# Optimization experiments

Hardware: AMD Instinct MI355X
Metric: run time of the kernel (lower is better)

The kernel has to match this reference:

```python
import jax, jax.numpy as jnp
import numpy as np

N_OBJ = 4096
IN_DIM = 1024
OUT_DIM = 1024
H = OUT_DIM // 2  # per-direction hidden, BidirectionalTreeLSTM uses out_dim//2
L = 2             # num_layer


def _build_tree(n):
    # balanced binary heap tree: node i has children 2i+1, 2i+2
    left = np.array([2 * i + 1 if 2 * i + 1 < n else -1 for i in range(n)], np.int32)
    right = np.array([2 * i + 2 if 2 * i + 2 < n else -1 for i in range(n)], np.int32)
    parent = np.full(n, -1, np.int32)
    for i in range(n):
        if left[i] >= 0:
            parent[left[i]] = i
        if right[i] >= 0:
            parent[right[i]] = i
    post, stack = [], [(0, False)]
    while stack:
        node, seen = stack.pop()
        if node < 0:
            continue
        if seen:
            post.append(node)
        else:
            stack.append((node, True))
            stack.append((int(right[node]), False))
            stack.append((int(left[node]), False))
    pre, stack = [], [0]
    while stack:
        node = stack.pop()
        if node < 0:
            continue
        pre.append(node)
        stack.append(int(right[node]))
        stack.append(int(left[node]))
    pad = lambda a: np.where(a < 0, n, a).astype(np.int32)  # slot n = zeros (no child/parent)
    return (np.array(post, np.int32), np.array(pre, np.int32),
            pad(left), pad(right), pad(parent))


def setup_inputs() -> dict:
    key = jax.random.key(0)
    ks = jax.random.split(key, 8)
    post, pre, left, right, parent = _build_tree(N_OBJ)

    def w(k, shape, fan_in):
        return jax.random.normal(k, shape, jnp.float32) * np.float32(1.0 / np.sqrt(fan_in))

    # bias init per the torch module: forget-gate blocks get constants, rest zero
    fw_bl = np.zeros((L, 6 * H), np.float32); fw_bl[:, 2 * H:4 * H] = 0.5
    fw_br = fw_bl.copy()
    bw_bh = np.zeros((L, 5 * H), np.float32); bw_bh[:, 2 * H:3 * H] = 1.0

    return {
        "features": jax.random.normal(ks[0], (N_OBJ, IN_DIM), jnp.float32),
        "fw_Wp": w(ks[1], (L, H, IN_DIM), IN_DIM),
        "fw_bp": jnp.zeros((L, H), jnp.float32),
        "fw_Wx": w(ks[2], (L, 6 * H, IN_DIM), IN_DIM),
        "fw_bx": jnp.zeros((L, 6 * H), jnp.float32),
        "fw_Wl": w(ks[3], (L, 6 * H, H), H),
        "fw_bl": jnp.asarray(fw_bl),
        "fw_Wr": w(ks[4], (L, 6 * H, H), H),
        "fw_br": jnp.asarray(fw_br),
        "bw_Wp": w(ks[5], (L, H, IN_DIM), IN_DIM),
        "bw_bp": jnp.zeros((L, H), jnp.float32),
        "bw_Wx": w(ks[6], (L, 5 * H, IN_DIM), IN_DIM),
        "bw_bx": jnp.zeros((L, 5 * H), jnp.float32),
        "bw_Wh": w(ks[7], (L, 5 * H, H), H),
        "bw_bh": jnp.asarray(bw_bh),
        "post_order": jnp.asarray(post),
        "pre_order": jnp.asarray(pre),
        "left_child": jnp.asarray(left),
        "right_child": jnp.asarray(right),
        "parent": jnp.asarray(parent),
    }


def _tree_leaves_to_root(feats, Wp, bp, Wx, bx, Wl, bl, Wr, br,
                         post_order, left_child, right_child):
    n = feats.shape[0]
    h = bp.shape[0]
    px = feats @ Wp.T + bp   # [n, h]   -- self path
    x2 = feats @ Wx.T + bx   # [n, 6h]  -- gate input, batched once

    def step(carry, idx):
        cbuf, hbuf = carry   # [n+1, h]; row n is permanent zero slot for missing children
        lc = left_child[idx]
        rc = right_child[idx]
        g = x2[idx] + hbuf[lc] @ Wl.T + bl + hbuf[rc] @ Wr.T + br
        i, o, fl, fr, u, r = jnp.split(g, 6)
        i = jax.nn.sigmoid(i); o = jax.nn.sigmoid(o)
        fl = jax.nn.sigmoid(fl); fr = jax.nn.sigmoid(fr)
        u = jnp.tanh(u); r = jax.nn.sigmoid(r)
        c = i * u + fl * cbuf[lc] + fr * cbuf[rc]
        hc = o * jnp.tanh(c)
        hf = r * hc + (1.0 - r) * px[idx]   # highway mix
        return (cbuf.at[idx].set(c), hbuf.at[idx].set(hf)), None

    init = (jnp.zeros((n + 1, h), feats.dtype), jnp.zeros((n + 1, h), feats.dtype))
    (_, hbuf), _ = jax.lax.scan(step, init, post_order)
    return hbuf[:n]


def _tree_root_to_leaves(feats, Wp, bp, Wx, bx, Wh, bh, pre_order, parent):
    n = feats.shape[0]
    h = bp.shape[0]
    px = feats @ Wp.T + bp   # [n, h]
    x2 = feats @ Wx.T + bx   # [n, 5h]

    def step(carry, idx):
        cbuf, hbuf = carry
        p = parent[idx]      # root maps to zero slot n -> iofuh(0) == bias, as in torch
        g = x2[idx] + hbuf[p] @ Wh.T + bh
        i, o, f, u, r = jnp.split(g, 5)
        i = jax.nn.sigmoid(i); o = jax.nn.sigmoid(o)
        f = jax.nn.sigmoid(f); u = jnp.tanh(u); r = jax.nn.sigmoid(r)
        c = i * u + f * cbuf[p]
        hc = o * jnp.tanh(c)
        hf = r * hc + (1.0 - r) * px[idx]
        return (cbuf.at[idx].set(c), hbuf.at[idx].set(hf)), None

    init = (jnp.zeros((n + 1, h), feats.dtype), jnp.zeros((n + 1, h), feats.dtype))
    (_, hbuf), _ = jax.lax.scan(step, init, pre_order)
    return hbuf[:n]


def reference(features, fw_Wp, fw_bp, fw_Wx, fw_bx, fw_Wl, fw_bl, fw_Wr, fw_br,
              bw_Wp, bw_bp, bw_Wx, bw_bx, bw_Wh, bw_bh,
              post_order, pre_order, left_child, right_child, parent):
    feats = features
    for l in range(L):  # MultiLayer_BTreeLSTM: stacked bidirectional layers
        h_fwd = _tree_leaves_to_root(feats, fw_Wp[l], fw_bp[l], fw_Wx[l], fw_bx[l],
                                     fw_Wl[l], fw_bl[l], fw_Wr[l], fw_br[l],
                                     post_order, left_child, right_child)
        h_bwd = _tree_root_to_leaves(feats, bw_Wp[l], bw_bp[l], bw_Wx[l], bw_bx[l],
                                     bw_Wh[l], bw_bh[l], pre_order, parent)
        feats = jnp.concatenate([h_fwd, h_bwd], axis=1)  # [n, out_dim]
    return feats
```

## Files before the change

kernel.cpp:

```cpp
#include <hip/hip_runtime.h>
#include <cstdint>
#include <cstddef>


#define HDIM 512
#define ZROW 4096
#define NCAT 6656

typedef _Float16 f16;
typedef f16   f16x8 __attribute__((ext_vector_type(8)));
typedef float f32x4 __attribute__((ext_vector_type(4)));

__device__ __forceinline__ float sigm(float x) { return 1.0f / (1.0f + expf(-x)); }

__device__ __forceinline__ void glds16(const f16* g, f16* l)
{
    __builtin_amdgcn_global_load_lds(
        (const __attribute__((address_space(1))) void*)g,
        (__attribute__((address_space(3))) void*)l,
        16, 0, 0);
}

__global__ __launch_bounds__(256) void cvt16(
    const float* __restrict__ s, f16* __restrict__ d, int n8)
{
    int i = blockIdx.x * 256 + threadIdx.x;
    if (i >= n8) return;
    float4 v0 = ((const float4*)s)[(size_t)i * 2];
    float4 v1 = ((const float4*)s)[(size_t)i * 2 + 1];
    f16x8 o;
    o[0] = (f16)v0.x; o[1] = (f16)v0.y; o[2] = (f16)v0.z; o[3] = (f16)v0.w;
    o[4] = (f16)v1.x; o[5] = (f16)v1.y; o[6] = (f16)v1.z; o[7] = (f16)v1.w;
    *(f16x8*)(d + (size_t)i * 8) = o;
}

__global__ __launch_bounds__(256) void cvt16_lr(
    const float* __restrict__ Wl, const float* __restrict__ Wr, f16* __restrict__ d)
{
    int i = blockIdx.x * 256 + threadIdx.x;
    int col8 = (i * 8) & 1023;
    int row  = (i * 8) >> 10;
    const float* s = (col8 < HDIM) ? (Wl + (size_t)row * HDIM + col8)
                                   : (Wr + (size_t)row * HDIM + col8 - HDIM);
    float4 v0 = ((const float4*)s)[0];
    float4 v1 = ((const float4*)s)[1];
    f16x8 o;
    o[0] = (f16)v0.x; o[1] = (f16)v0.y; o[2] = (f16)v0.z; o[3] = (f16)v0.w;
    o[4] = (f16)v1.x; o[5] = (f16)v1.y; o[6] = (f16)v1.z; o[7] = (f16)v1.w;
    int np = (row & 511) * 6 + (row >> 9);
    *(f16x8*)(d + (size_t)np * 1024 + col8) = o;
}

__global__ __launch_bounds__(256) void cvt16_perm5(
    const float* __restrict__ s, f16* __restrict__ d)
{
    int i = blockIdx.x * 256 + threadIdx.x;
    int col8 = (i * 8) & 511;
    int row  = (i * 8) >> 9;
    float4 v0 = ((const float4*)(s + (size_t)row * HDIM + col8))[0];
    float4 v1 = ((const float4*)(s + (size_t)row * HDIM + col8))[1];
    f16x8 o;
    o[0] = (f16)v0.x; o[1] = (f16)v0.y; o[2] = (f16)v0.z; o[3] = (f16)v0.w;
    o[4] = (f16)v1.x; o[5] = (f16)v1.y; o[6] = (f16)v1.z; o[7] = (f16)v1.w;
    int np = (row & 511) * 5 + (row >> 9);
    *(f16x8*)(d + (size_t)np * HDIM + col8) = o;
}

__global__ __launch_bounds__(256) void biascat_k(
    const float* __restrict__ a, const float* __restrict__ b,
    const float* __restrict__ c, const float* __restrict__ dd,
    float* __restrict__ o)
{
    int t = blockIdx.x * 256 + threadIdx.x;
    if (t >= NCAT) return;
    float v;
    if (t < 512) v = a[t];
    else if (t < 3584) v = b[t - 512];
    else if (t < 4096) v = c[t - 3584];
    else v = dd[t - 4096];
    o[t] = v;
}

__global__ void zero_slots(f16* H, float* cbf, float* cbb)
{
    int t = threadIdx.x;
    H[(size_t)ZROW * 1024 + t] = (f16)0.0f;
    if (t < HDIM) {
        cbf[(size_t)ZROW * HDIM + t] = 0.0f;
        cbb[(size_t)ZROW * HDIM + t] = 0.0f;
    }
}

__global__ __launch_bounds__(256) void mm_pre(
    const f16* __restrict__ A, const f16* __restrict__ W,
    const float* __restrict__ bias, f16* __restrict__ C, int N, int K)
{
    __shared__ __align__(16) f16 Ab[2][128 * 32];
    __shared__ __align__(16) f16 Bb[2][128 * 32];
    const int t  = threadIdx.x;
    const int L  = t & 63;
    const int w  = t >> 6;
    const int wm = (w & 1) << 6;
    const int wn = (w >> 1) << 6;
    const int fr = L & 15;
    const int fq = L >> 4;
    const int la  = L >> 2;
    const int cs  = (((L & 3) ^ ((L >> 3) & 3)) << 3);

    const f16* a0 = A + (size_t)(blockIdx.y * 128 + w * 16 + la) * K + cs;
    const f16* a1 = a0 + (size_t)64 * K;
    const f16* b0 = W + (size_t)(blockIdx.x * 128 + w * 16 + la) * K + cs;
    const f16* b1 = b0 + (size_t)64 * K;
    const int lo = w * 512 + L * 8;
    const int hi = lo + 2048;

    f32x4 acc[4][4] = {};
    const int nt = K >> 5;

#define STG_P(sel, k0)                       \
    do {                                     \
        glds16(a0 + (k0), &Ab[sel][lo]);     \
        glds16(a1 + (k0), &Ab[sel][hi]);     \
        glds16(b0 + (k0), &Bb[sel][lo]);     \
        glds16(b1 + (k0), &Bb[sel][hi]);     \
    } while (0)

    STG_P(0, 0);
    __syncthreads();
    int cur = 0;
    const int fsw = ((fr >> 1) & 3) << 3;
    for (int tt = 0; tt < nt; ++tt) {
        if (tt + 1 < nt) STG_P(cur ^ 1, (tt + 1) << 5);
        f16x8 af[4], bg[4];
#pragma unroll
        for (int i = 0; i < 4; ++i)
            af[i] = *(const f16x8*)(&Ab[cur][(wm + i * 16 + fr) * 32 + ((fq << 3) ^ fsw)]);
#pragma unroll
        for (int j = 0; j < 4; ++j)
            bg[j] = *(const f16x8*)(&Bb[cur][(wn + j * 16 + fr) * 32 + ((fq << 3) ^ fsw)]);
#pragma unroll
        for (int i = 0; i < 4; ++i)
#pragma unroll
            for (int j = 0; j < 4; ++j)
                acc[i][j] = __builtin_amdgcn_mfma_f32_16x16x32_f16(
                    af[i], bg[j], acc[i][j], 0, 0, 0);
        __syncthreads();
        cur ^= 1;
    }
#undef STG_P

    const int gr0 = blockIdx.y * 128 + wm + fq * 4;
    const int gc0 = blockIdx.x * 128 + wn + fr;
#pragma unroll
    for (int j = 0; j < 4; ++j) {
        const int gc = gc0 + j * 16;
        const float bj = bias[gc];
#pragma unroll
        for (int i = 0; i < 4; ++i) {
            const int gr = gr0 + i * 16;
#pragma unroll
            for (int rr = 0; rr < 4; ++rr)
                C[(size_t)(gr + rr) * N + gc] = (f16)(acc[i][j][rr] + bj);
        }
    }
}

__global__ __launch_bounds__(256) void stage_fused(
    const f16* __restrict__ Wlr, const f16* __restrict__ Wh,
    f16* H, const f16* __restrict__ PX,
    const int* __restrict__ lc, const int* __restrict__ rc,
    const int* __restrict__ par,
    int fbase, int fm, int bbase, int bm,
    float* __restrict__ cbf, float* __restrict__ cbb,
    float* out32,
    const float* __restrict__ bl, const float* __restrict__ br,
    const float* __restrict__ bh)
{
    __shared__ __align__(16) char smem[57344];
    f16*   Ab0 = (f16*)smem;
    f16*   Bb0 = (f16*)(smem + 32768);
    float* Sg  = (float*)smem;

    const int t   = threadIdx.x;
    const int L   = t & 63;
    const int w   = t >> 6;
    const int fr  = L & 15;
    const int fq  = L >> 4;
    const int rch = L >> 3;
    const int cs  = (((L & 7) ^ rch) << 3);
    const int fsw = (fr & 7) << 3;
    const int nfB = ((fm + 127) >> 7) * 32;

    if ((int)blockIdx.x < nfB) {
        const int by = blockIdx.x >> 5;
        const int bx = blockIdx.x & 31;
        const int wm = (w & 1) << 6;
        const int wn = (w >> 1) * 48;

        const f16* aLo[4]; const f16* aHi[4];
#pragma unroll
        for (int cc = 0; cc < 4; ++cc) {
            int g  = by * 128 + (w * 4 + cc) * 8 + rch;
            int n1 = ZROW, n2 = ZROW;
            if (g < fm) { n1 = lc[fbase + g]; n2 = rc[fbase + g]; }
            aLo[cc] = H + (size_t)n1 * 1024 + cs;
            aHi[cc] = H + (size_t)n2 * 1024 + cs - HDIM;
        }
        const f16* bsrc[3];
#pragma unroll
        for (int cc = 0; cc < 3; ++cc)
            bsrc[cc] = Wlr + (size_t)(bx * 96 + (w * 3 + cc) * 8 + rch) * 1024 + cs;

        f32x4 acc[4][3] = {};
#define STGF(sel, k0)                                                        \
        do {                                                                 \
            const bool hiK = (k0) >= HDIM;                                   \
            _Pragma("unroll")                                                \
            for (int cc = 0; cc < 4; ++cc)                                   \
                glds16((hiK ? aHi[cc] : aLo[cc]) + (k0),                     \
                       Ab0 + (sel) * 8192 + (w * 4 + cc) * 512 + L * 8);     \
            _Pragma("unroll")                                                \
            for (int cc = 0; cc < 3; ++cc)                                   \
                glds16(bsrc[cc] + (k0),                                      \
                       Bb0 + (sel) * 6144 + (w * 3 + cc) * 512 + L * 8);     \
        } while (0)

        STGF(0, 0);
        __syncthreads();
        int cur = 0;
        for (int tt = 0; tt < 16; ++tt) {
            if (tt + 1 < 16) STGF(cur ^ 1, (tt + 1) * 64);
            const f16* Ac = Ab0 + cur * 8192;
            const f16* Bc = Bb0 + cur * 6144;
            f16x8 af[4][2], bg[3][2];
#pragma unroll
            for (int i = 0; i < 4; ++i)
#pragma unroll
                for (int ks = 0; ks < 2; ++ks)
                    af[i][ks] = *(const f16x8*)(Ac + (wm + i * 16 + fr) * 64
                                + ((((ks * 4 + fq) << 3) ^ fsw)));
#pragma unroll
            for (int j = 0; j < 3; ++j)
#pragma unroll
                for (int ks = 0; ks < 2; ++ks)
                    bg[j][ks] = *(const f16x8*)(Bc + (wn + j * 16 + fr) * 64
                                + ((((ks * 4 + fq) << 3) ^ fsw)));
#pragma unroll
            for (int ks = 0; ks < 2; ++ks)
#pragma unroll
                for (int i = 0; i < 4; ++i)
#pragma unroll
                    for (int j = 0; j < 3; ++j)
                        acc[i][j] = __builtin_amdgcn_mfma_f32_16x16x32_f16(
                            af[i][ks], bg[j][ks], acc[i][j], 0, 0, 0);
            __syncthreads();
            cur ^= 1;
        }
#undef STGF
#pragma unroll
        for (int i = 0; i < 4; ++i)
#pragma unroll
            for (int j = 0; j < 3; ++j)
#pragma unroll
                for (int rr = 0; rr < 4; ++rr)
                    Sg[(wm + i * 16 + fq * 4 + rr) * 100 + wn + j * 16 + fr]
                        = acc[i][j][rr];
        __syncthreads();
        const int rmax = fm - by * 128;
        const int j0 = bx * 16;
        for (int cc = 0; cc < 8; ++cc) {
            int cell = t + cc * 256;
            int r = cell >> 4, j = cell & 15;
            if (r >= rmax) break;
            int node = fbase + by * 128 + r;
            int jj = j0 + j;
            const f16* pxr = PX + (size_t)node * NCAT;
            float g[6];
#pragma unroll
            for (int q = 0; q < 6; ++q)
                g[q] = (float)pxr[HDIM + q * HDIM + jj] + bl[q * HDIM + jj]
                     + br[q * HDIM + jj] + Sg[r * 100 + j * 6 + q];
            int lcn = lc[node], rcn = rc[node];
            float clv = cbf[(size_t)lcn * HDIM + jj];
            float crv = cbf[(size_t)rcn * HDIM + jj];
            float i_ = sigm(g[0]), o_ = sigm(g[1]), fl_ = sigm(g[2]), fr_ = sigm(g[3]);
            float u_ = tanhf(g[4]), r_ = sigm(g[5]);
            float c  = i_ * u_ + fl_ * clv + fr_ * crv;
            float hc = o_ * tanhf(c);
            float px = (float)pxr[jj];
            float hf = r_ * hc + (1.0f - r_) * px;
            cbf[(size_t)node * HDIM + jj] = c;
            H[(size_t)node * 1024 + jj] = (f16)hf;
            if (out32) out32[(size_t)node * 1024 + jj] = hf;
        }
    } else {
        const int b2 = blockIdx.x - nfB;
        const int by = b2 >> 5;
        const int bx = b2 & 31;
        const int wm = w * 32;

        const f16* asrc[4];
#pragma unroll
        for (int cc = 0; cc < 4; ++cc) {
            int g = by * 128 + (w * 4 + cc) * 8 + rch;
            int n1 = ZROW;
            if (g < bm) n1 = par[bbase + g];
            asrc[cc] = H + (size_t)n1 * 1024 + HDIM + cs;
        }
        const f16* bsrc[3];
        int nbch[3];
#pragma unroll
        for (int cc = 0; cc < 3; ++cc) {
            int ch = w * 3 + cc;
            nbch[cc] = ch;
            bsrc[cc] = Wh + (size_t)(bx * 80 + ch * 8 + rch) * HDIM + cs;
        }

        f32x4 acc[2][5] = {};
#define STGB(sel, k0)                                                        \
        do {                                                                 \
            _Pragma("unroll")                                                \
            for (int cc = 0; cc < 4; ++cc)                                   \
                glds16(asrc[cc] + (k0),                                      \
                       Ab0 + (sel) * 8192 + (w * 4 + cc) * 512 + L * 8);     \
            _Pragma("unroll")                                                \
            for (int cc = 0; cc < 3; ++cc)                                   \
                if (nbch[cc] < 10)                                           \
                    glds16(bsrc[cc] + (k0),                                  \
                           Bb0 + (sel) * 5120 + nbch[cc] * 512 + L * 8);     \
        } while (0)

        STGB(0, 0);
        __syncthreads();
        int cur = 0;
        for (int tt = 0; tt < 8; ++tt) {
            if (tt + 1 < 8) STGB(cur ^ 1, (tt + 1) * 64);
            const f16* Ac = Ab0 + cur * 8192;
            const f16* Bc = Bb0 + cur * 5120;
            f16x8 af[2][2], bg[5][2];
#pragma unroll
            for (int i = 0; i < 2; ++i)
#pragma unroll
                for (int ks = 0; ks < 2; ++ks)
                    af[i][ks] = *(const f16x8*)(Ac + (wm + i * 16 + fr) * 64
                                + ((((ks * 4 + fq) << 3) ^ fsw)));
#pragma unroll
            for (int j = 0; j < 5; ++j)
#pragma unroll
                for (int ks = 0; ks < 2; ++ks)
                    bg[j][ks] = *(const f16x8*)(Bc + (j * 16 + fr) * 64
                                + ((((ks * 4 + fq) << 3) ^ fsw)));
#pragma unroll
            for (int ks = 0; ks < 2; ++ks)
#pragma unroll
                for (int i = 0; i < 2; ++i)
#pragma unroll
                    for (int j = 0; j < 5; ++j)
                        acc[i][j] = __builtin_amdgcn_mfma_f32_16x16x32_f16(
                            af[i][ks], bg[j][ks], acc[i][j], 0, 0, 0);
            __syncthreads();
            cur ^= 1;
        }
#undef STGB
#pragma unroll
        for (int i = 0; i < 2; ++i)
#pragma unroll
            for (int j = 0; j < 5; ++j)
#pragma unroll
                for (int rr = 0; rr < 4; ++rr)
                    Sg[(wm + i * 16 + fq * 4 + rr) * 84 + j * 16 + fr]
                        = acc[i][j][rr];
        __syncthreads();
        const int rmax = bm - by * 128;
        const int j0 = bx * 16;
        for (int cc = 0; cc < 8; ++cc) {
            int cell = t + cc * 256;
            int r = cell >> 4, j = cell & 15;
            if (r >= rmax) break;
            int node = bbase + by * 128 + r;
            int jj = j0 + j;
            const f16* pxr = PX + (size_t)node * NCAT;
            float g[5];
#pragma unroll
            for (int q = 0; q < 5; ++q)
                g[q] = (float)pxr[4096 + q * HDIM + jj] + bh[q * HDIM + jj]
                     + Sg[r * 84 + j * 5 + q];
            int p = par[node];
            float cp = cbb[(size_t)p * HDIM + jj];
            float i_ = sigm(g[0]), o_ = sigm(g[1]), f_ = sigm(g[2]);
            float u_ = tanhf(g[3]), r_ = sigm(g[4]);
            float c  = i_ * u_ + f_ * cp;
            float hc = o_ * tanhf(c);
            float px = (float)pxr[3584 + jj];
            float hf = r_ * hc + (1.0f - r_) * px;
            cbb[(size_t)node * HDIM + jj] = c;
            H[(size_t)node * 1024 + HDIM + jj] = (f16)hf;
            if (out32) out32[(size_t)node * 1024 + HDIM + jj] = hf;
        }
    }
}

__global__ __launch_bounds__(256) void elem_merged(
    const f16* __restrict__ PX,
    int fbase, int fm, int bbase, int bm,
    const int* __restrict__ lc, const int* __restrict__ rc,
    const int* __restrict__ par,
    float* __restrict__ cbf, float* __restrict__ cbb,
    f16* __restrict__ H, float* __restrict__ out32,
    const float* __restrict__ bl, const float* __restrict__ br,
    const float* __restrict__ bh)
{
    int t = blockIdx.x * 256 + threadIdx.x;
    const int fvec = fm * 64;
    if (t < fvec) {
        int row = t >> 6, j8 = (t & 63) << 3;
        int node = fbase + row;
        const f16* pxr = PX + (size_t)node * NCAT;
        float g[6][8];
#pragma unroll
        for (int q = 0; q < 6; ++q) {
            f16x8 pv = *(const f16x8*)(pxr + HDIM + q * HDIM + j8);
            const float* blp = bl + q * HDIM + j8;
            const float* brp = br + q * HDIM + j8;
#pragma unroll
            for (int e = 0; e < 8; ++e)
                g[q][e] = (float)pv[e] + blp[e] + brp[e];
        }
        int lcn = lc[node], rcn = rc[node];
        const float* clp = cbf + (size_t)lcn * HDIM + j8;
        const float* crp = cbf + (size_t)rcn * HDIM + j8;
        f32x4 cl0 = *(const f32x4*)clp, cl1 = *(const f32x4*)(clp + 4);
        f32x4 cr0 = *(const f32x4*)crp, cr1 = *(const f32x4*)(crp + 4);
        f16x8 pxv = *(const f16x8*)(pxr + j8);
        f32x4 co0, co1;
        f16x8 hv;
        f32x4 ho0, ho1;
#pragma unroll
        for (int e = 0; e < 8; ++e) {
            float clv = (e < 4) ? cl0[e & 3] : cl1[e & 3];
            float crv = (e < 4) ? cr0[e & 3] : cr1[e & 3];
            float i_ = sigm(g[0][e]), o_ = sigm(g[1][e]);
            float fl_ = sigm(g[2][e]), fr_ = sigm(g[3][e]);
            float u_ = tanhf(g[4][e]), r_ = sigm(g[5][e]);
            float c  = i_ * u_ + fl_ * clv + fr_ * crv;
            float hc = o_ * tanhf(c);
            float hf = r_ * hc + (1.0f - r_) * (float)pxv[e];
            if (e < 4) { co0[e & 3] = c; ho0[e & 3] = hf; }
            else       { co1[e & 3] = c; ho1[e & 3] = hf; }
            hv[e] = (f16)hf;
        }
        float* cdst = cbf + (size_t)node * HDIM + j8;
        *(f32x4*)cdst = co0; *(f32x4*)(cdst + 4) = co1;
        *(f16x8*)(H + (size_t)node * 1024 + j8) = hv;
        if (out32) {
            float* od = out32 + (size_t)node * 1024 + j8;
            *(f32x4*)od = ho0; *(f32x4*)(od + 4) = ho1;
        }
    } else {
        int t2 = t - fvec;
        if (t2 >= bm * 64) return;
        int row = t2 >> 6, j8 = (t2 & 63) << 3;
        int node = bbase + row;
        const f16* pxr = PX + (size_t)node * NCAT;
        float g[5][8];
#pragma unroll
        for (int q = 0; q < 5; ++q) {
            f16x8 pv = *(const f16x8*)(pxr + 4096 + q * HDIM + j8);
            const float* bhp = bh + q * HDIM + j8;
#pragma unroll
            for (int e = 0; e < 8; ++e)
                g[q][e] = (float)pv[e] + bhp[e];
        }
        int p = par[node];
        const float* cpp = cbb + (size_t)p * HDIM + j8;
        f32x4 cp0 = *(const f32x4*)cpp, cp1 = *(const f32x4*)(cpp + 4);
        f16x8 pxv = *(const f16x8*)(pxr + 3584 + j8);
        f32x4 co0, co1;
        f16x8 hv;
        f32x4 ho0, ho1;
#pragma unroll
        for (int e = 0; e < 8; ++e) {
            float cpv = (e < 4) ? cp0[e & 3] : cp1[e & 3];
            float i_ = sigm(g[0][e]), o_ = sigm(g[1][e]), f_ = sigm(g[2][e]);
            float u_ = tanhf(g[3][e]), r_ = sigm(g[4][e]);
            float c  = i_ * u_ + f_ * cpv;
            float hc = o_ * tanhf(c);
            float hf = r_ * hc + (1.0f - r_) * (float)pxv[e];
            if (e < 4) { co0[e & 3] = c; ho0[e & 3] = hf; }
            else       { co1[e & 3] = c; ho1[e & 3] = hf; }
            hv[e] = (f16)hf;
        }
        float* cdst = cbb + (size_t)node * HDIM + j8;
        *(f32x4*)cdst = co0; *(f32x4*)(cdst + 4) = co1;
        *(f16x8*)(H + (size_t)node * 1024 + HDIM + j8) = hv;
        if (out32) {
            float* od = out32 + (size_t)node * 1024 + HDIM + j8;
            *(f32x4*)od = ho0; *(f32x4*)(od + 4) = ho1;
        }
    }
}

extern "C" void kernel_launch(void* const* d_in, const int* in_sizes, int n_in,
                              void* d_out, int out_size, void* d_ws, size_t ws_size,
                              hipStream_t stream)
{
    (void)in_sizes; (void)n_in; (void)out_size; (void)ws_size;
    const float* features = (const float*)d_in[0];
    const float* fw_Wp = (const float*)d_in[1];
    const float* fw_bp = (const float*)d_in[2];
    const float* fw_Wx = (const float*)d_in[3];
    const float* fw_bx = (const float*)d_in[4];
    const float* fw_Wl = (const float*)d_in[5];
    const float* fw_bl = (const float*)d_in[6];
    const float* fw_Wr = (const float*)d_in[7];
    const float* fw_br = (const float*)d_in[8];
    const float* bw_Wp = (const float*)d_in[9];
    const float* bw_bp = (const float*)d_in[10];
    const float* bw_Wx = (const float*)d_in[11];
    const float* bw_bx = (const float*)d_in[12];
    const float* bw_Wh = (const float*)d_in[13];
    const float* bw_bh = (const float*)d_in[14];
    const int* lc  = (const int*)d_in[17];
    const int* rc  = (const int*)d_in[18];
    const int* par = (const int*)d_in[19];

    f16* feat16 = (f16*)d_ws;
    f16* H      = feat16 + (size_t)4096 * 1024;
    f16* Wcat   = H     + (size_t)4097 * 1024;
    f16* Wlr    = Wcat  + (size_t)NCAT * 1024;
    f16* Wh     = Wlr   + (size_t)3072 * 1024;
    f16* PX     = Wh    + (size_t)2560 * 512;
    float* biascat = (float*)(PX + (size_t)4096 * NCAT);
    float* cbf     = biascat + NCAT;
    float* cbb     = cbf + (size_t)4097 * HDIM;

    zero_slots<<<dim3(1), dim3(1024), 0, stream>>>(H, cbf, cbb);
    cvt16<<<dim3(2048), 256, 0, stream>>>(features, feat16, 4096 * 1024 / 8);

    static const int fb[12] = {2047, 1023, 511, 255, 127, 63, 31, 15, 7, 3, 1, 0};
    static const int fmv[12] = {1, 1024, 512, 256, 128, 64, 32, 16, 8, 4, 2, 1};
    static const int bb[12] = {1, 3, 7, 15, 31, 63, 127, 255, 511, 1023, 2047, 4095};
    static const int bmv[12] = {2, 4, 8, 16, 32, 64, 128, 256, 512, 1024, 2048, 1};

    for (int l = 0; l < 2; ++l) {
        cvt16<<<dim3(256),  256, 0, stream>>>(fw_Wp + (size_t)l * 512 * 1024,  Wcat,               512 * 1024 / 8);
        cvt16<<<dim3(1536), 256, 0, stream>>>(fw_Wx + (size_t)l * 3072 * 1024, Wcat + 512 * 1024,  3072 * 1024 / 8);
        cvt16<<<dim3(256),  256, 0, stream>>>(bw_Wp + (size_t)l * 512 * 1024,  Wcat + 3584 * 1024, 512 * 1024 / 8);
        cvt16<<<dim3(1280), 256, 0, stream>>>(bw_Wx + (size_t)l * 2560 * 1024, Wcat + (size_t)4096 * 1024, 2560 * 1024 / 8);
        cvt16_lr<<<dim3(1536), 256, 0, stream>>>(fw_Wl + (size_t)l * 3072 * 512,
                                                 fw_Wr + (size_t)l * 3072 * 512, Wlr);
        cvt16_perm5<<<dim3(640), 256, 0, stream>>>(bw_Wh + (size_t)l * 2560 * 512, Wh);
        biascat_k<<<dim3(26), 256, 0, stream>>>(fw_bp + (size_t)l * 512, fw_bx + (size_t)l * 3072,
                                                bw_bp + (size_t)l * 512, bw_bx + (size_t)l * 2560, biascat);

        const f16* A16 = (l == 0) ? feat16 : H;
        mm_pre<<<dim3(NCAT / 128, 4096 / 128), 256, 0, stream>>>(
            A16, Wcat, biascat, PX, NCAT, 1024);

        float* o32 = (l == 1) ? (float*)d_out : nullptr;
        const float* bl_l = fw_bl + (size_t)l * 3072;
        const float* br_l = fw_br + (size_t)l * 3072;
        const float* bh_l = bw_bh + (size_t)l * 2560;

        {
            int tot = (2048 + 1) * 64;
            elem_merged<<<dim3((tot + 255) / 256), 256, 0, stream>>>(
                PX, 2048, 2048, 0, 1,
                lc, rc, par, cbf, cbb, H, o32, bl_l, br_l, bh_l);
        }
        for (int i = 0; i < 12; ++i) {
            int nfB = ((fmv[i] + 127) >> 7) * 32;
            int nbB = ((bmv[i] + 127) >> 7) * 32;
            stage_fused<<<dim3(nfB + nbB), 256, 0, stream>>>(
                Wlr, Wh, H, PX, lc, rc, par,
                fb[i], fmv[i], bb[i], bmv[i],
                cbf, cbb, o32, bl_l, br_l, bh_l);
        }
    }
}
```

Before: 838.1 us.

## Software-pipeline MFMA GEMM loops with explicit waitcnt and interleaved LDS loads

Reworks the inner loops of mm_pre, the forward-stage and the backward-stage GEMMs. The one __syncthreads per iteration becomes an explicit vmcnt wait plus barrier, and LDS fragment reads are interleaved with MFMA groups under partial lgkmcnt waits and sched_barriers. This is meant to overlap LDS reads, global-to-LDS prefetch issue and matrix math. mm_pre also doubles its K tile to 64 with a new swizzle, which doubles its LDS use. Hand-written waitcnt counts risk hazards if the compiler's instruction counts differ from the assumed ones.

```diff
diff --git a/kernel.cpp b/kernel.cpp
--- a/kernel.cpp
+++ b/kernel.cpp
@@ -20,6 +20,13 @@
         (__attribute__((address_space(3))) void*)l,
         16, 0, 0);
 }
+
+#define WAIT_VM0()  do { asm volatile("s_waitcnt vmcnt(0)" ::: "memory"); \
+                         __builtin_amdgcn_sched_barrier(0); } while (0)
+#define WAIT_LG(n)  do { asm volatile("s_waitcnt lgkmcnt(" #n ")" ::: "memory"); \
+                         __builtin_amdgcn_sched_barrier(0); } while (0)
+#define BARRIER()   do { __builtin_amdgcn_s_barrier(); \
+                         __builtin_amdgcn_sched_barrier(0); } while (0)
 
 __global__ __launch_bounds__(256) void cvt16(
     const float* __restrict__ s, f16* __restrict__ d, int n8)
@@ -95,8 +102,8 @@
     const f16* __restrict__ A, const f16* __restrict__ W,
     const float* __restrict__ bias, f16* __restrict__ C, int N, int K)
 {
-    __shared__ __align__(16) f16 Ab[2][128 * 32];
-    __shared__ __align__(16) f16 Bb[2][128 * 32];
+    __shared__ __align__(16) f16 Ab[2][128 * 64];
+    __shared__ __align__(16) f16 Bb[2][128 * 64];
     const int t  = threadIdx.x;
     const int L  = t & 63;
     const int w  = t >> 6;
@@ -104,50 +111,73 @@
     const int wn = (w >> 1) << 6;
     const int fr = L & 15;
     const int fq = L >> 4;
-    const int la  = L >> 2;
-    const int cs  = (((L & 3) ^ ((L >> 3) & 3)) << 3);
-
-    const f16* a0 = A + (size_t)(blockIdx.y * 128 + w * 16 + la) * K + cs;
-    const f16* a1 = a0 + (size_t)64 * K;
-    const f16* b0 = W + (size_t)(blockIdx.x * 128 + w * 16 + la) * K + cs;
-    const f16* b1 = b0 + (size_t)64 * K;
-    const int lo = w * 512 + L * 8;
-    const int hi = lo + 2048;
+    const int rch = L >> 3;
+    const int cs  = (((L & 7) ^ rch) << 3);
+    const int fsw = (fr & 7) << 3;
+
+    const f16* ap[4]; const f16* bp[4];
+#pragma unroll
+    for (int cc = 0; cc < 4; ++cc) {
+        ap[cc] = A + (size_t)(blockIdx.y * 128 + (w * 4 + cc) * 8 + rch) * K + cs;
+        bp[cc] = W + (size_t)(blockIdx.x * 128 + (w * 4 + cc) * 8 + rch) * K + cs;
+    }
+
+#define STG2(sel, k0, p)                                                   \
+    do {                                                                   \
+        glds16(ap[p] + (k0), &Ab[sel][(w * 4 + (p)) * 512 + L * 8]);       \
+        glds16(bp[p] + (k0), &Bb[sel][(w * 4 + (p)) * 512 + L * 8]);       \
+    } while (0)
 
     f32x4 acc[4][4] = {};
-    const int nt = K >> 5;
-
-#define STG_P(sel, k0)                       \
-    do {                                     \
-        glds16(a0 + (k0), &Ab[sel][lo]);     \
-        glds16(a1 + (k0), &Ab[sel][hi]);     \
-        glds16(b0 + (k0), &Bb[sel][lo]);     \
-        glds16(b1 + (k0), &Bb[sel][hi]);     \
+    f16x8 af0[2][2], bg0[2][2], af1[2][2], bg1[2][2];
+
+#define LDQ(AF, BG, cur, qi, qj)                                                   \
+    do {                                                                           \
+        _Pragma("unroll") for (int i2 = 0; i2 < 2; ++i2)                           \
+        _Pragma("unroll") for (int ks = 0; ks < 2; ++ks) {                         \
+            AF[i2][ks] = *(const f16x8*)(&Ab[cur][(wm + ((qi)*2+i2)*16 + fr)*64    \
+                         + ((((ks*4+fq) << 3) ^ fsw))]);                           \
+            BG[i2][ks] = *(const f16x8*)(&Bb[cur][(wn + ((qj)*2+i2)*16 + fr)*64    \
+                         + ((((ks*4+fq) << 3) ^ fsw))]);                           \
+        }                                                                          \
     } while (0)
 
-    STG_P(0, 0);
-    __syncthreads();
-    int cur = 0;
-    const int fsw = ((fr >> 1) & 3) << 3;
+#define MFQ(AF, BG, qi, qj)                                                        \
+    do {                                                                           \
+        _Pragma("unroll") for (int ks = 0; ks < 2; ++ks)                           \
+        _Pragma("unroll") for (int i2 = 0; i2 < 2; ++i2)                           \
+        _Pragma("unroll") for (int j2 = 0; j2 < 2; ++j2)                           \
+            acc[(qi)*2+i2][(qj)*2+j2] = __builtin_amdgcn_mfma_f32_16x16x32_f16(    \
+                AF[i2][ks], BG[j2][ks], acc[(qi)*2+i2][(qj)*2+j2], 0, 0, 0);       \
+    } while (0)
+
+    const int nt = K >> 6;
+    STG2(0, 0, 0); STG2(0, 0, 1); STG2(0, 0, 2); STG2(0, 0, 3);
     for (int tt = 0; tt < nt; ++tt) {
-        if (tt + 1 < nt) STG_P(cur ^ 1, (tt + 1) << 5);
-        f16x8 af[4], bg[4];
-#pragma unroll
-        for (int i = 0; i < 4; ++i)
-            af[i] = *(const f16x8*)(&Ab[cur][(wm + i * 16 + fr) * 32 + ((fq << 3) ^ fsw)]);
-#pragma unroll
-        for (int j = 0; j < 4; ++j)
-            bg[j] = *(const f16x8*)(&Bb[cur][(wn + j * 16 + fr) * 32 + ((fq << 3) ^ fsw)]);
-#pragma unroll
-        for (int i = 0; i < 4; ++i)
-#pragma unroll
-            for (int j = 0; j < 4; ++j)
-                acc[i][j] = __builtin_amdgcn_mfma_f32_16x16x32_f16(
-                    af[i], bg[j], acc[i][j], 0, 0, 0);
-        __syncthreads();
-        cur ^= 1;
+        const int cur = tt & 1;
+        const int kn  = (tt + 1) << 6;
+        const bool pf = (tt + 1 < nt);
+        WAIT_VM0();
+        BARRIER();
+        LDQ(af0, bg0, cur, 0, 0);
+        LDQ(af1, bg1, cur, 0, 1);
+        if (pf) STG2(cur ^ 1, kn, 0);
+        WAIT_LG(8);
+        MFQ(af0, bg0, 0, 0);
+        LDQ(af0, bg0, cur, 1, 0);
+        if (pf) STG2(cur ^ 1, kn, 1);
+        WAIT_LG(8);
+        MFQ(af1, bg1, 0, 1);
+        LDQ(af1, bg1, cur, 1, 1);
+        if (pf) { STG2(cur ^ 1, kn, 2); STG2(cur ^ 1, kn, 3); }
+        WAIT_LG(8);
+        MFQ(af0, bg0, 1, 0);
+        WAIT_LG(0);
+        MFQ(af1, bg1, 1, 1);
     }
-#undef STG_P
+#undef STG2
+#undef LDQ
+#undef MFQ
 
     const int gr0 = blockIdx.y * 128 + wm + fq * 4;
     const int gc0 = blockIdx.x * 128 + wn + fr;
@@ -212,51 +242,72 @@
             bsrc[cc] = Wlr + (size_t)(bx * 96 + (w * 3 + cc) * 8 + rch) * 1024 + cs;
 
         f32x4 acc[4][3] = {};
-#define STGF(sel, k0)                                                        \
+        f16x8 af[4][2], bgA[2], bgB[2], bgC[2];
+
+#define STGF_A(sel, k0)                                                      \
         do {                                                                 \
             const bool hiK = (k0) >= HDIM;                                   \
             _Pragma("unroll")                                                \
             for (int cc = 0; cc < 4; ++cc)                                   \
                 glds16((hiK ? aHi[cc] : aLo[cc]) + (k0),                     \
                        Ab0 + (sel) * 8192 + (w * 4 + cc) * 512 + L * 8);     \
+        } while (0)
+#define STGF_B(sel, k0)                                                      \
+        do {                                                                 \
             _Pragma("unroll")                                                \
             for (int cc = 0; cc < 3; ++cc)                                   \
                 glds16(bsrc[cc] + (k0),                                      \
                        Bb0 + (sel) * 6144 + (w * 3 + cc) * 512 + L * 8);     \
         } while (0)
-
-        STGF(0, 0);
+#define LDAF(cur)                                                            \
+        do {                                                                 \
+            const f16* Ac = Ab0 + (cur) * 8192;                              \
+            _Pragma("unroll") for (int i = 0; i < 4; ++i)                    \
+            _Pragma("unroll") for (int ks = 0; ks < 2; ++ks)                 \
+                af[i][ks] = *(const f16x8*)(Ac + (wm + i * 16 + fr) * 64     \
+                            + ((((ks * 4 + fq) << 3) ^ fsw)));               \
+        } while (0)
+#define LDBG(BG, cur, j)                                                     \
+        do {                                                                 \
+            const f16* Bc = Bb0 + (cur) * 6144;                              \
+            _Pragma("unroll") for (int ks = 0; ks < 2; ++ks)                 \
+                BG[ks] = *(const f16x8*)(Bc + (wn + (j) * 16 + fr) * 64      \
+                            + ((((ks * 4 + fq) << 3) ^ fsw)));               \
+        } while (0)
+#define MFJ(BG, j)                                                           \
+        do {                                                                 \
+            _Pragma("unroll") for (int ks = 0; ks < 2; ++ks)                 \
+            _Pragma("unroll") for (int i = 0; i < 4; ++i)                    \
+                acc[i][j] = __builtin_amdgcn_mfma_f32_16x16x32_f16(          \
+                    af[i][ks], BG[ks], acc[i][j], 0, 0, 0);                  \
+        } while (0)
+
+        STGF_A(0, 0); STGF_B(0, 0);
+        for (int tt = 0; tt < 16; ++tt) {
+            const int cur = tt & 1;
+            const int kn  = (tt + 1) * 64;
+            const bool pf = (tt < 15);
+            WAIT_VM0();
+            BARRIER();
+            LDAF(cur);
+            LDBG(bgA, cur, 0);
+            LDBG(bgB, cur, 1);
+            if (pf) STGF_A(cur ^ 1, kn);
+            WAIT_LG(2);
+            MFJ(bgA, 0);
+            LDBG(bgC, cur, 2);
+            if (pf) STGF_B(cur ^ 1, kn);
+            WAIT_LG(2);
+            MFJ(bgB, 1);
+            WAIT_LG(0);
+            MFJ(bgC, 2);
+        }
+#undef STGF_A
+#undef STGF_B
+#undef LDAF
+#undef LDBG
+#undef MFJ
         __syncthreads();
-        int cur = 0;
-        for (int tt = 0; tt < 16; ++tt) {
-            if (tt + 1 < 16) STGF(cur ^ 1, (tt + 1) * 64);
-            const f16* Ac = Ab0 + cur * 8192;
-            const f16* Bc = Bb0 + cur * 6144;
-            f16x8 af[4][2], bg[3][2];
-#pragma unroll
-            for (int i = 0; i < 4; ++i)
-#pragma unroll
-                for (int ks = 0; ks < 2; ++ks)
-                    af[i][ks] = *(const f16x8*)(Ac + (wm + i * 16 + fr) * 64
-                                + ((((ks * 4 + fq) << 3) ^ fsw)));
-#pragma unroll
-            for (int j = 0; j < 3; ++j)
-#pragma unroll
-                for (int ks = 0; ks < 2; ++ks)
-                    bg[j][ks] = *(const f16x8*)(Bc + (wn + j * 16 + fr) * 64
-                                + ((((ks * 4 + fq) << 3) ^ fsw)));
-#pragma unroll
-            for (int ks = 0; ks < 2; ++ks)
-#pragma unroll
-                for (int i = 0; i < 4; ++i)
-#pragma unroll
-                    for (int j = 0; j < 3; ++j)
-                        acc[i][j] = __builtin_amdgcn_mfma_f32_16x16x32_f16(
-                            af[i][ks], bg[j][ks], acc[i][j], 0, 0, 0);
-            __syncthreads();
-            cur ^= 1;
-        }
-#undef STGF
 #pragma unroll
         for (int i = 0; i < 4; ++i)
 #pragma unroll
@@ -317,51 +368,78 @@
         }
 
         f32x4 acc[2][5] = {};
-#define STGB(sel, k0)                                                        \
+        f16x8 af[2][2], bg0[2], bg1[2], bg2[2], bg3[2], bg4[2];
+
+#define STGB_A(sel, k0)                                                      \
         do {                                                                 \
             _Pragma("unroll")                                                \
             for (int cc = 0; cc < 4; ++cc)                                   \
                 glds16(asrc[cc] + (k0),                                      \
                        Ab0 + (sel) * 8192 + (w * 4 + cc) * 512 + L * 8);     \
+        } while (0)
+#define STGB_B(sel, k0)                                                      \
+        do {                                                                 \
             _Pragma("unroll")                                                \
             for (int cc = 0; cc < 3; ++cc)                                   \
                 if (nbch[cc] < 10)                                           \
                     glds16(bsrc[cc] + (k0),                                  \
                            Bb0 + (sel) * 5120 + nbch[cc] * 512 + L * 8);     \
         } while (0)
-
-        STGB(0, 0);
+#define LDAFB(cur)                                                           \
+        do {                                                                 \
+            const f16* Ac = Ab0 + (cur) * 8192;                              \
+            _Pragma("unroll") for (int i = 0; i < 2; ++i)                    \
+            _Pragma("unroll") for (int ks = 0; ks < 2; ++ks)                 \
+                af[i][ks] = *(const f16x8*)(Ac + (wm + i * 16 + fr) * 64     \
+                            + ((((ks * 4 + fq) << 3) ^ fsw)));               \
+        } while (0)
+#define LDBGB(BG, cur, j)                                                    \
+        do {                                                                 \
+            const f16* Bc = Bb0 + (cur) * 5120;                              \
+            _Pragma("unroll") for (int ks = 0; ks < 2; ++ks)                 \
+                BG[ks] = *(const f16x8*)(Bc + ((j) * 16 + fr) * 64           \
+                            + ((((ks * 4 + fq) << 3) ^ fsw)));               \
+        } while (0)
+#define MFJB(BG, j)                                                          \
+        do {                                                                 \
+            _Pragma("unroll") for (int ks = 0; ks < 2; ++ks)                 \
+            _Pragma("unroll") for (int i = 0; i < 2; ++i)                    \
+                acc[i][j] = __builtin_amdgcn_mfma_f32_16x16x32_f16(          \
+                    af[i][ks], BG[ks], acc[i][j], 0, 0, 0);                  \
+        } while (0)
+
+        STGB_A(0, 0); STGB_B(0, 0);
+        for (int tt = 0; tt < 8; ++tt) {
+            const int cur = tt & 1;
+            const int kn  = (tt + 1) * 64;
+            const bool pf = (tt < 7);
+            WAIT_VM0();
+            BARRIER();
+            LDAFB(cur);
+            LDBGB(bg0, cur, 0);
+            LDBGB(bg1, cur, 1);
+            if (pf) STGB_A(cur ^ 1, kn);
+            WAIT_LG(2);
+            MFJB(bg0, 0);
+            LDBGB(bg2, cur, 2);
+            if (pf) STGB_B(cur ^ 1, kn);
+            WAIT_LG(2);
+            MFJB(bg1, 1);
+            LDBGB(bg3, cur, 3);
+            WAIT_LG(2);
+            MFJB(bg2, 2);
+            LDBGB(bg4, cur, 4);
+            WAIT_LG(2);
+            MFJB(bg3, 3);
+            WAIT_LG(0);
+            MFJB(bg4, 4);
+        }
+#undef STGB_A
+#undef STGB_B
+#undef LDAFB
+#undef LDBGB
+#undef MFJB
         __syncthreads();
-        int cur = 0;
-        for (int tt = 0; tt < 8; ++tt) {
-            if (tt + 1 < 8) STGB(cur ^ 1, (tt + 1) * 64);
-            const f16* Ac = Ab0 + cur * 8192;
-            const f16* Bc = Bb0 + cur * 5120;
-            f16x8 af[2][2], bg[5][2];
-#pragma unroll
-            for (int i = 0; i < 2; ++i)
-#pragma unroll
-                for (int ks = 0; ks < 2; ++ks)
-                    af[i][ks] = *(const f16x8*)(Ac + (wm + i * 16 + fr) * 64
-                                + ((((ks * 4 + fq) << 3) ^ fsw)));
-#pragma unroll
-            for (int j = 0; j < 5; ++j)
-#pragma unroll
-                for (int ks = 0; ks < 2; ++ks)
-                    bg[j][ks] = *(const f16x8*)(Bc + (j * 16 + fr) * 64
-                                + ((((ks * 4 + fq) << 3) ^ fsw)));
-#pragma unroll
-            for (int ks = 0; ks < 2; ++ks)
-#pragma unroll
-                for (int i = 0; i < 2; ++i)
-#pragma unroll
-                    for (int j = 0; j < 5; ++j)
-                        acc[i][j] = __builtin_amdgcn_mfma_f32_16x16x32_f16(
-                            af[i][ks], bg[j][ks], acc[i][j], 0, 0, 0);
-            __syncthreads();
-            cur ^= 1;
-        }
-#undef STGB
 #pragma unroll
         for (int i = 0; i < 2; ++i)
 #pragma unroll
```

Result: slower. 868.3 us (+3.6%).

## Fuse per-layer weight conversions into one kernel and triple-buffer mm_pre loads

Applied to the files above, without the earlier changes.

Seven per-layer conversion and bias-concatenation launches are merged into a single prep_layer kernel that picks its role from the block index, cutting launch overhead. The projection GEMM mm_pre moves from double to triple buffering of shared-memory tiles. It prefetches two K-steps ahead and uses explicit vmcnt waits with a single barrier per iteration instead of two __syncthreads. This raises LDS use to 48KB per block, which may lower occupancy.

```diff
diff --git a/kernel.cpp b/kernel.cpp
--- a/kernel.cpp
+++ b/kernel.cpp
@@ -21,64 +21,79 @@
         16, 0, 0);
 }
 
-__global__ __launch_bounds__(256) void cvt16(
-    const float* __restrict__ s, f16* __restrict__ d, int n8)
-{
-    int i = blockIdx.x * 256 + threadIdx.x;
-    if (i >= n8) return;
-    float4 v0 = ((const float4*)s)[(size_t)i * 2];
-    float4 v1 = ((const float4*)s)[(size_t)i * 2 + 1];
-    f16x8 o;
-    o[0] = (f16)v0.x; o[1] = (f16)v0.y; o[2] = (f16)v0.z; o[3] = (f16)v0.w;
-    o[4] = (f16)v1.x; o[5] = (f16)v1.y; o[6] = (f16)v1.z; o[7] = (f16)v1.w;
-    *(f16x8*)(d + (size_t)i * 8) = o;
-}
-
-__global__ __launch_bounds__(256) void cvt16_lr(
-    const float* __restrict__ Wl, const float* __restrict__ Wr, f16* __restrict__ d)
-{
-    int i = blockIdx.x * 256 + threadIdx.x;
-    int col8 = (i * 8) & 1023;
-    int row  = (i * 8) >> 10;
-    const float* s = (col8 < HDIM) ? (Wl + (size_t)row * HDIM + col8)
-                                   : (Wr + (size_t)row * HDIM + col8 - HDIM);
+#define WAIT_VM4()  do { asm volatile("s_waitcnt vmcnt(4)" ::: "memory"); \
+                         __builtin_amdgcn_sched_barrier(0); } while (0)
+#define WAIT_VM0()  do { asm volatile("s_waitcnt vmcnt(0)" ::: "memory"); \
+                         __builtin_amdgcn_sched_barrier(0); } while (0)
+#define BARRIER()   do { __builtin_amdgcn_s_barrier(); \
+                         __builtin_amdgcn_sched_barrier(0); } while (0)
+
+__device__ __forceinline__ void cvt8s(const float* __restrict__ s, f16* __restrict__ d)
+{
     float4 v0 = ((const float4*)s)[0];
     float4 v1 = ((const float4*)s)[1];
     f16x8 o;
     o[0] = (f16)v0.x; o[1] = (f16)v0.y; o[2] = (f16)v0.z; o[3] = (f16)v0.w;
     o[4] = (f16)v1.x; o[5] = (f16)v1.y; o[6] = (f16)v1.z; o[7] = (f16)v1.w;
-    int np = (row & 511) * 6 + (row >> 9);
-    *(f16x8*)(d + (size_t)np * 1024 + col8) = o;
-}
-
-__global__ __launch_bounds__(256) void cvt16_perm5(
-    const float* __restrict__ s, f16* __restrict__ d)
+    *(f16x8*)d = o;
+}
+
+__global__ __launch_bounds__(256) void cvt16(
+    const float* __restrict__ s, f16* __restrict__ d, int n8)
 {
     int i = blockIdx.x * 256 + threadIdx.x;
-    int col8 = (i * 8) & 511;
-    int row  = (i * 8) >> 9;
-    float4 v0 = ((const float4*)(s + (size_t)row * HDIM + col8))[0];
-    float4 v1 = ((const float4*)(s + (size_t)row * HDIM + col8))[1];
-    f16x8 o;
-    o[0] = (f16)v0.x; o[1] = (f16)v0.y; o[2] = (f16)v0.z; o[3] = (f16)v0.w;
-    o[4] = (f16)v1.x; o[5] = (f16)v1.y; o[6] = (f16)v1.z; o[7] = (f16)v1.w;
-    int np = (row & 511) * 5 + (row >> 9);
-    *(f16x8*)(d + (size_t)np * HDIM + col8) = o;
-}
-
-__global__ __launch_bounds__(256) void biascat_k(
-    const float* __restrict__ a, const float* __restrict__ b,
-    const float* __restrict__ c, const float* __restrict__ dd,
-    float* __restrict__ o)
-{
-    int t = blockIdx.x * 256 + threadIdx.x;
-    if (t >= NCAT) return;
-    float v;
-    if (t < 512) v = a[t];
-    else if (t < 3584) v = b[t - 512];
-    else if (t < 4096) v = c[t - 3584];
-    else v = dd[t - 4096];
-    o[t] = v;
+    if (i >= n8) return;
+    cvt8s(s + (size_t)i * 8, d + (size_t)i * 8);
+}
+
+__global__ __launch_bounds__(256) void prep_layer(
+    const float* __restrict__ fWp, const float* __restrict__ fWx,
+    const float* __restrict__ bWp, const float* __restrict__ bWx,
+    const float* __restrict__ fWl, const float* __restrict__ fWr,
+    const float* __restrict__ bWh,
+    const float* __restrict__ fbp, const float* __restrict__ fbx,
+    const float* __restrict__ bbp, const float* __restrict__ bbx,
+    f16* __restrict__ Wcat, f16* __restrict__ Wlr, f16* __restrict__ Wh,
+    float* __restrict__ biascat)
+{
+    const int bid = blockIdx.x;
+    const int t   = threadIdx.x;
+    if (bid < 256) {
+        int i = bid * 256 + t;
+        cvt8s(fWp + (size_t)i * 8, Wcat + (size_t)i * 8);
+    } else if (bid < 1792) {
+        int i = (bid - 256) * 256 + t;
+        cvt8s(fWx + (size_t)i * 8, Wcat + (size_t)512 * 1024 + (size_t)i * 8);
+    } else if (bid < 2048) {
+        int i = (bid - 1792) * 256 + t;
+        cvt8s(bWp + (size_t)i * 8, Wcat + (size_t)3584 * 1024 + (size_t)i * 8);
+    } else if (bid < 3328) {
+        int i = (bid - 2048) * 256 + t;
+        cvt8s(bWx + (size_t)i * 8, Wcat + (size_t)4096 * 1024 + (size_t)i * 8);
+    } else if (bid < 4864) {
+        int i = (bid - 3328) * 256 + t;
+        int col8 = (i * 8) & 1023;
+        int row  = (i * 8) >> 10;
+        const float* s = (col8 < HDIM) ? (fWl + (size_t)row * HDIM + col8)
+                                       : (fWr + (size_t)row * HDIM + col8 - HDIM);
+        int np = (row & 511) * 6 + (row >> 9);
+        cvt8s(s, Wlr + (size_t)np * 1024 + col8);
+    } else if (bid < 5504) {
+        int i = (bid - 4864) * 256 + t;
+        int col8 = (i * 8) & 511;
+        int row  = (i * 8) >> 9;
+        int np = (row & 511) * 5 + (row >> 9);
+        cvt8s(bWh + (size_t)row * HDIM + col8, Wh + (size_t)np * HDIM + col8);
+    } else {
+        int i = (bid - 5504) * 256 + t;
+        if (i >= NCAT) return;
+        float v;
+        if (i < 512) v = fbp[i];
+        else if (i < 3584) v = fbx[i - 512];
+        else if (i < 4096) v = bbp[i - 3584];
+        else v = bbx[i - 4096];
+        biascat[i] = v;
+    }
 }
 
 __global__ void zero_slots(f16* H, float* cbf, float* cbb)
@@ -95,8 +110,8 @@
     const f16* __restrict__ A, const f16* __restrict__ W,
     const float* __restrict__ bias, f16* __restrict__ C, int N, int K)
 {
-    __shared__ __align__(16) f16 Ab[2][128 * 32];
-    __shared__ __align__(16) f16 Bb[2][128 * 32];
+    __shared__ __align__(16) f16 Ab[3][128 * 32];
+    __shared__ __align__(16) f16 Bb[3][128 * 32];
     const int t  = threadIdx.x;
     const int L  = t & 63;
     const int w  = t >> 6;
@@ -116,6 +131,7 @@
 
     f32x4 acc[4][4] = {};
     const int nt = K >> 5;
+    const int fsw = ((fr >> 1) & 3) << 3;
 
 #define STG_P(sel, k0)                       \
     do {                                     \
@@ -126,11 +142,12 @@
     } while (0)
 
     STG_P(0, 0);
-    __syncthreads();
-    int cur = 0;
-    const int fsw = ((fr >> 1) & 3) << 3;
+    STG_P(1, 32);
+    int cur = 0, nxt2 = 2;
     for (int tt = 0; tt < nt; ++tt) {
-        if (tt + 1 < nt) STG_P(cur ^ 1, (tt + 1) << 5);
+        if (tt + 2 < nt) { WAIT_VM4(); } else { WAIT_VM0(); }
+        BARRIER();
+        if (tt + 2 < nt) STG_P(nxt2, (tt + 2) << 5);
         f16x8 af[4], bg[4];
 #pragma unroll
         for (int i = 0; i < 4; ++i)
@@ -144,8 +161,8 @@
             for (int j = 0; j < 4; ++j)
                 acc[i][j] = __builtin_amdgcn_mfma_f32_16x16x32_f16(
                     af[i], bg[j], acc[i][j], 0, 0, 0);
-        __syncthreads();
-        cur ^= 1;
+        cur = (cur == 2) ? 0 : cur + 1;
+        nxt2 = (nxt2 == 2) ? 0 : nxt2 + 1;
     }
 #undef STG_P
 
@@ -348,7 +365,7 @@
             for (int j = 0; j < 5; ++j)
 #pragma unroll
                 for (int ks = 0; ks < 2; ++ks)
-                    bg[j][ks] = *(const f16x8*)(Bc + (j * 16 + fr) * 64
+                    bg[j][ks] = *(const f16x8*)(Bc + ((j) * 16 + fr) * 64
                                 + ((((ks * 4 + fq) << 3) ^ fsw)));
 #pragma unroll
             for (int ks = 0; ks < 2; ++ks)
@@ -543,15 +560,14 @@
     static const int bmv[12] = {2, 4, 8, 16, 32, 64, 128, 256, 512, 1024, 2048, 1};
 
     for (int l = 0; l < 2; ++l) {
-        cvt16<<<dim3(256),  256, 0, stream>>>(fw_Wp + (size_t)l * 512 * 1024,  Wcat,               512 * 1024 / 8);
-        cvt16<<<dim3(1536), 256, 0, stream>>>(fw_Wx + (size_t)l * 3072 * 1024, Wcat + 512 * 1024,  3072 * 1024 / 8);
-        cvt16<<<dim3(256),  256, 0, stream>>>(bw_Wp + (size_t)l * 512 * 1024,  Wcat + 3584 * 1024, 512 * 1024 / 8);
-        cvt16<<<dim3(1280), 256, 0, stream>>>(bw_Wx + (size_t)l * 2560 * 1024, Wcat + (size_t)4096 * 1024, 2560 * 1024 / 8);
-        cvt16_lr<<<dim3(1536), 256, 0, stream>>>(fw_Wl + (size_t)l * 3072 * 512,
-                                                 fw_Wr + (size_t)l * 3072 * 512, Wlr);
-        cvt16_perm5<<<dim3(640), 256, 0, stream>>>(bw_Wh + (size_t)l * 2560 * 512, Wh);
-        biascat_k<<<dim3(26), 256, 0, stream>>>(fw_bp + (size_t)l * 512, fw_bx + (size_t)l * 3072,
-                                                bw_bp + (size_t)l * 512, bw_bx + (size_t)l * 2560, biascat);
+        prep_layer<<<dim3(5530), 256, 0, stream>>>(
+            fw_Wp + (size_t)l * 512 * 1024,  fw_Wx + (size_t)l * 3072 * 1024,
+            bw_Wp + (size_t)l * 512 * 1024,  bw_Wx + (size_t)l * 2560 * 1024,
+            fw_Wl + (size_t)l * 3072 * 512,  fw_Wr + (size_t)l * 3072 * 512,
+            bw_Wh + (size_t)l * 2560 * 512,
+            fw_bp + (size_t)l * 512, fw_bx + (size_t)l * 3072,
+            bw_bp + (size_t)l * 512, bw_bx + (size_t)l * 2560,
+            Wcat, Wlr, Wh, biascat);
 
         const f16* A16 = (l == 0) ? feat16 : H;
         mm_pre<<<dim3(NCAT / 128, 4096 / 128), 256, 0, stream>>>(
```

Result: faster. 795.1 us (-5.1%).
